# Kernel optimization log

Hardware: AMD Instinct MI355X
Metric: run time of the kernel (lower is better)

## Reference

```python
import jax, jax.numpy as jnp
import numpy as np

D = 1024
E = 8


def setup_inputs() -> dict:
    key = jax.random.key(0)
    ks = jax.random.split(key, 7)
    s = 1.0 / np.sqrt(D)
    x = jax.random.normal(ks[0], (4, 2048, D), dtype=jnp.float32)
    Wg = jax.random.uniform(ks[1], (D, E), minval=-s, maxval=s, dtype=jnp.float32)
    bg = jax.random.uniform(ks[2], (E,), minval=-s, maxval=s, dtype=jnp.float32)
    W1 = jax.random.uniform(ks[3], (E, D, D), minval=-s, maxval=s, dtype=jnp.float32)
    b1 = jax.random.uniform(ks[4], (E, D), minval=-s, maxval=s, dtype=jnp.float32)
    W2 = jax.random.uniform(ks[5], (E, D, D), minval=-s, maxval=s, dtype=jnp.float32)
    b2 = jax.random.uniform(ks[6], (E, D), minval=-s, maxval=s, dtype=jnp.float32)
    return {"x": x, "Wg": Wg, "bg": bg, "W1": W1, "b1": b1, "W2": W2, "b2": b2}


def reference(x, Wg, bg, W1, b1, W2, b2):
    N, T, d = x.shape
    x_flat = x.reshape(N * T, d)                                  # [NT, D]
    logits = x_flat @ Wg + bg                                     # [NT, E]
    probs = jax.nn.softmax(logits, axis=-1)
    assignments = jnp.argmax(probs, axis=-1)                      # [NT]
    # all-experts MLP (dense, as in the original module)
    h = jnp.einsum('nd,edh->neh', x_flat, W1) + b1[None]          # [NT, E, D]
    h = jax.nn.gelu(h, approximate=False)                         # torch GELU = exact erf
    eo = jnp.einsum('neh,ehd->ned', h, W2) + b2[None]             # [NT, E, D]
    selected = jnp.take_along_axis(eo, assignments[:, None, None], axis=1)[:, 0, :]  # [NT, D]
    w = jnp.take_along_axis(probs, assignments[:, None], axis=1)  # [NT, 1]
    out = (w * selected).reshape(N, T, d)
    return out
```

## Files before the change

### kernel.cpp

```cpp
#include <hip/hip_runtime.h>
#include <cstdint>

#define NT 8192
#define DD 1024
#define NE 8
#define BK 32
#define NKIT (DD / BK)
#define TM 64
#define MAXTILE 136

typedef __attribute__((ext_vector_type(8))) _Float16 half8;
typedef __attribute__((ext_vector_type(4))) float f32x4;

__device__ __forceinline__ unsigned short f2h_bits(float f) {
  _Float16 h = (_Float16)f;
  return __builtin_bit_cast(unsigned short, h);
}

#define GLDS16(gp, lp) __builtin_amdgcn_global_load_lds( \
  (__attribute__((address_space(1))) void*)(uintptr_t)(gp), \
  (__attribute__((address_space(3))) void*)(uintptr_t)(lp), 16, 0, 0)

#define WAITCNT_VM6  0xF76
#define WAITCNT_VM3  0xF73
#define WAITCNT_VM0  0xF70

__global__ __launch_bounds__(256) void wcast_kernel(
    const float* __restrict__ W1, const float* __restrict__ W2,
    _Float16* __restrict__ W1t, _Float16* __restrict__ W2t) {
  __shared__ float tile[64][65];
  const int z = blockIdx.z;
  const float* W = (z < 8 ? W1 : W2) + (size_t)(z & 7) * (DD * DD);
  _Float16* Wt   = (z < 8 ? W1t : W2t) + (size_t)(z & 7) * (DD * DD);
  const int k0 = blockIdx.x * 64, n0 = blockIdx.y * 64;
  const int tid = threadIdx.x;
#pragma unroll
  for (int it = 0; it < 4; ++it) {
    int idx = it * 256 + tid;
    int r = idx >> 4;
    int q = idx & 15;
    float4 v = *(const float4*)(W + (size_t)(k0 + r) * DD + n0 + q * 4);
    tile[r][q * 4 + 0] = v.x; tile[r][q * 4 + 1] = v.y;
    tile[r][q * 4 + 2] = v.z; tile[r][q * 4 + 3] = v.w;
  }
  __syncthreads();
#pragma unroll
  for (int it = 0; it < 4; ++it) {
    int idx = it * 256 + tid;
    int n = idx >> 4;
    int q = idx & 15;
    ushort4 o;
    o.x = f2h_bits(tile[q * 4 + 0][n]);
    o.y = f2h_bits(tile[q * 4 + 1][n]);
    o.z = f2h_bits(tile[q * 4 + 2][n]);
    o.w = f2h_bits(tile[q * 4 + 3][n]);
    *(ushort4*)(Wt + (size_t)(n0 + n) * DD + k0 + q * 4) = o;
  }
}

__global__ __launch_bounds__(256) void gate_kernel(
    const float* __restrict__ x, const float* __restrict__ Wg, const float* __restrict__ bg,
    int* __restrict__ assign, float* __restrict__ wgt, _Float16* __restrict__ xh) {
  __shared__ float WgL[NE * DD];
  const int tid = threadIdx.x;
#pragma unroll
  for (int it = 0; it < 8; ++it) {
    int idx = it * 256 + tid;
    float4 v = ((const float4*)Wg)[idx];
    int k = idx >> 1;
    int e0 = (idx & 1) * 4;
    WgL[(e0 + 0) * DD + k] = v.x;
    WgL[(e0 + 1) * DD + k] = v.y;
    WgL[(e0 + 2) * DD + k] = v.z;
    WgL[(e0 + 3) * DD + k] = v.w;
  }
  __syncthreads();
  const int lane = tid & 63, w = tid >> 6;
#pragma unroll
  for (int s = 0; s < 2; ++s) {
    const int t = blockIdx.x * 8 + w * 2 + s;
    const float4* xr = (const float4*)(x + (size_t)t * DD);
    float4 xv[4];
#pragma unroll
    for (int c = 0; c < 4; ++c) xv[c] = xr[lane + 64 * c];
    ushort4* xo = (ushort4*)(xh + (size_t)t * DD);
#pragma unroll
    for (int c = 0; c < 4; ++c) {
      union { ushort4 u; _Float16 h[4]; } cv;
      cv.h[0] = (_Float16)xv[c].x; cv.h[1] = (_Float16)xv[c].y;
      cv.h[2] = (_Float16)xv[c].z; cv.h[3] = (_Float16)xv[c].w;
      xo[lane + 64 * c] = cv.u;
    }
    float p[NE];
#pragma unroll
    for (int e = 0; e < NE; ++e) {
      float acc = 0.f;
#pragma unroll
      for (int c = 0; c < 4; ++c) {
        float4 wv = *(const float4*)&WgL[e * DD + 4 * lane + 256 * c];
        acc += xv[c].x * wv.x + xv[c].y * wv.y + xv[c].z * wv.z + xv[c].w * wv.w;
      }
      p[e] = acc;
    }
#pragma unroll
    for (int e = 0; e < NE; ++e) {
      float v = p[e];
      for (int off = 32; off > 0; off >>= 1) v += __shfl_down(v, off, 64);
      p[e] = v;
    }
    if (lane == 0) {
      float l[NE];
#pragma unroll
      for (int e = 0; e < NE; ++e) l[e] = p[e] + bg[e];
      int a = 0; float best = l[0];
#pragma unroll
      for (int e = 1; e < NE; ++e) if (l[e] > best) { best = l[e]; a = e; }
      float sum = 0.f;
#pragma unroll
      for (int e = 0; e < NE; ++e) sum += expf(l[e] - best);
      assign[t] = a;
      wgt[t] = 1.0f / sum;
    }
  }
}

__global__ __launch_bounds__(1024) void sort_kernel(
    const int* __restrict__ assign, int* __restrict__ rowtok, int* __restrict__ plan) {
  __shared__ int sc[NE * 1024];
  __shared__ int s_pref[NE + 1];
  const int tid = threadIdx.x;
  int a[8];
  int c[NE];
#pragma unroll
  for (int e = 0; e < NE; ++e) c[e] = 0;
#pragma unroll
  for (int j = 0; j < 8; ++j) { a[j] = assign[tid * 8 + j]; ++c[a[j]]; }
#pragma unroll
  for (int e = 0; e < NE; ++e) sc[e * 1024 + tid] = c[e];
  __syncthreads();
  for (int d = 1; d < 1024; d <<= 1) {
    int add[NE];
    if (tid >= d) {
#pragma unroll
      for (int e = 0; e < NE; ++e) add[e] = sc[e * 1024 + tid - d];
    }
    __syncthreads();
    if (tid >= d) {
#pragma unroll
      for (int e = 0; e < NE; ++e) sc[e * 1024 + tid] += add[e];
    }
    __syncthreads();
  }
  int tot[NE], incl[NE];
#pragma unroll
  for (int e = 0; e < NE; ++e) { tot[e] = sc[e * 1024 + 1023]; incl[e] = sc[e * 1024 + tid]; }
  int offs[NE];
  {
    int s = 0;
#pragma unroll
    for (int e = 0; e < NE; ++e) { offs[e] = s; s += tot[e]; }
  }
  int run[NE];
#pragma unroll
  for (int e = 0; e < NE; ++e) run[e] = offs[e] + incl[e] - c[e];
#pragma unroll
  for (int j = 0; j < 8; ++j) { int e = a[j]; rowtok[run[e]++] = tid * 8 + j; }
  if (tid == 0) {
    int s = 0;
    for (int e = 0; e < NE; ++e) { s_pref[e] = s; s += (tot[e] + TM - 1) / TM; }
    s_pref[NE] = s;
    plan[0] = s;
  }
  __syncthreads();
  const int nt = s_pref[NE];
  if (tid < nt) {
    int e = 0;
    while (tid >= s_pref[e + 1]) ++e;
    int t = tid - s_pref[e];
    plan[1 + tid] = e;
    plan[1 + MAXTILE + tid] = offs[e] + t * TM;
    plan[1 + 2 * MAXTILE + tid] = offs[e] + tot[e];
  }
}

template <int MODE>
__global__ __launch_bounds__(256) void gemm_kernel(
    const _Float16* __restrict__ A,
    const _Float16* __restrict__ Wt,
    const float* __restrict__ bias,
    const int* __restrict__ plan,
    _Float16* __restrict__ Hout,
    float* __restrict__ Fout,
    const int* __restrict__ rowtok,
    const float* __restrict__ wgt) {
  const int wrk = blockIdx.x;
  const int tile = wrk >> 3;
  if (tile >= plan[0]) return;
  const int e = plan[1 + tile];
  const int m0 = plan[1 + MAXTILE + tile];
  const int seg_end = plan[1 + 2 * MAXTILE + tile];
  const int n0 = (wrk & 7) * 128;

  const int tid = threadIdx.x;
  const int lane = tid & 63;
  const int wn = tid >> 6;
  const int quad = lane >> 4;
  const int r15 = lane & 15;

  __shared__ alignas(16) char lds[49152];

  const _Float16* We = Wt + (size_t)e * DD * DD;
  const _Float16* gAp;
  const _Float16* gBp[2];
  int ldsoA, ldsoB[2];
  {
    int slot = tid;
    int row = slot >> 2;
    int c = (slot & 3) ^ ((row >> 1) & 3);
    int rg = m0 + row; if (rg > NT - 1) rg = NT - 1;
    int arow = (MODE == 0) ? rowtok[rg] : rg;
    gAp = A + (size_t)arow * DD + c * 8;
    ldsoA = slot * 16;
  }
#pragma unroll
  for (int i = 0; i < 2; ++i) {
    int slot = i * 256 + tid;
    int row = slot >> 2;
    int c = (slot & 3) ^ ((row >> 1) & 3);
    gBp[i] = We + (size_t)(n0 + row) * DD + c * 8;
    ldsoB[i] = slot * 16;
  }

  int aoff[4], boff[2];
#pragma unroll
  for (int i = 0; i < 4; ++i) {
    int m = i * 16 + r15;
    aoff[i] = m * 4 + (quad ^ ((m >> 1) & 3));
  }
#pragma unroll
  for (int i = 0; i < 2; ++i) {
    int n = wn * 32 + i * 16 + r15;
    boff[i] = n * 4 + (quad ^ ((n >> 1) & 3));
  }

  f32x4 acc[4][2];
  f32x4 zero4 = {0.f, 0.f, 0.f, 0.f};
#pragma unroll
  for (int mi = 0; mi < 4; ++mi)
#pragma unroll
    for (int ni = 0; ni < 2; ++ni) acc[mi][ni] = zero4;

#define LDSBUF(B) (lds + (B) * 12288)
#define STAGE(KT, BUF) do {                                          \
    const int ko_ = (KT) * BK;                                       \
    char* lb_ = LDSBUF(BUF);                                         \
    GLDS16(gAp + ko_, lb_ + ldsoA);                                  \
    GLDS16(gBp[0] + ko_, lb_ + 4096 + ldsoB[0]);                     \
    GLDS16(gBp[1] + ko_, lb_ + 4096 + ldsoB[1]);                     \
  } while (0)
#define COMPUTE(BUF) do {                                            \
    const half8* AsV = (const half8*)(LDSBUF(BUF));                  \
    const half8* BsV = (const half8*)(LDSBUF(BUF) + 4096);           \
    half8 a_[4], b_[2];                                              \
    _Pragma("unroll")                                                \
    for (int i = 0; i < 4; ++i) a_[i] = AsV[aoff[i]];                \
    _Pragma("unroll")                                                \
    for (int i = 0; i < 2; ++i) b_[i] = BsV[boff[i]];                \
    _Pragma("unroll")                                                \
    for (int mi = 0; mi < 4; ++mi)                                   \
      _Pragma("unroll")                                              \
      for (int ni = 0; ni < 2; ++ni)                                 \
        acc[mi][ni] = __builtin_amdgcn_mfma_f32_16x16x32_f16(a_[mi], b_[ni], acc[mi][ni], 0, 0, 0); \
  } while (0)

  STAGE(0, 0);
  STAGE(1, 1);
  STAGE(2, 2);

#pragma unroll 1
  for (int kt = 0; kt < NKIT - 3; ++kt) {
    __builtin_amdgcn_s_waitcnt(WAITCNT_VM6);
    __builtin_amdgcn_s_barrier();
    __asm__ volatile("" ::: "memory");
    STAGE(kt + 3, (kt + 3) & 3);
    COMPUTE(kt & 3);
  }
  __builtin_amdgcn_s_waitcnt(WAITCNT_VM6);
  __builtin_amdgcn_s_barrier();
  __asm__ volatile("" ::: "memory");
  COMPUTE((NKIT - 3) & 3);
  __builtin_amdgcn_s_waitcnt(WAITCNT_VM3);
  __builtin_amdgcn_s_barrier();
  __asm__ volatile("" ::: "memory");
  COMPUTE((NKIT - 2) & 3);
  __builtin_amdgcn_s_waitcnt(WAITCNT_VM0);
  __builtin_amdgcn_s_barrier();
  __asm__ volatile("" ::: "memory");
  COMPUTE((NKIT - 1) & 3);
#undef COMPUTE
#undef STAGE
#undef LDSBUF

  const float* bptr = bias + (size_t)e * DD;
#pragma unroll
  for (int mi = 0; mi < 4; ++mi) {
    int rowb = m0 + mi * 16 + quad * 4;
#pragma unroll
    for (int r = 0; r < 4; ++r) {
      int gpos = rowb + r;
      if (gpos < seg_end) {
        if (MODE == 0) {
#pragma unroll
          for (int ni = 0; ni < 2; ++ni) {
            int n = n0 + wn * 32 + ni * 16 + r15;
            float val = acc[mi][ni][r] + bptr[n];
            val = 0.5f * val * (1.0f + erff(val * 0.70710678118654752f));
            Hout[(size_t)gpos * DD + n] = (_Float16)val;
          }
        } else {
          int tok = rowtok[gpos];
          float wv = wgt[tok];
          float* orow = Fout + (size_t)tok * DD;
#pragma unroll
          for (int ni = 0; ni < 2; ++ni) {
            int n = n0 + wn * 32 + ni * 16 + r15;
            orow[n] = (acc[mi][ni][r] + bptr[n]) * wv;
          }
        }
      }
    }
  }
}

extern "C" void kernel_launch(void* const* d_in, const int* in_sizes, int n_in,
                              void* d_out, int out_size, void* d_ws, size_t ws_size,
                              hipStream_t stream) {
  const float* x  = (const float*)d_in[0];
  const float* Wg = (const float*)d_in[1];
  const float* bg = (const float*)d_in[2];
  const float* W1 = (const float*)d_in[3];
  const float* b1 = (const float*)d_in[4];
  const float* W2 = (const float*)d_in[5];
  const float* b2 = (const float*)d_in[6];
  float* out = (float*)d_out;

  char* ws = (char*)d_ws;
  const size_t MB16 = (size_t)1 << 24;
  _Float16* W1t = (_Float16*)(ws + 0 * MB16);
  _Float16* W2t = (_Float16*)(ws + 1 * MB16);
  _Float16* xh  = (_Float16*)(ws + 2 * MB16);
  _Float16* H   = (_Float16*)(ws + 3 * MB16);
  int*   assign = (int*)(ws + 4 * MB16);
  int*   rowtok = assign + NT;
  float* wgt    = (float*)(rowtok + NT);
  int*   plan   = (int*)(wgt + NT);

  wcast_kernel<<<dim3(16, 16, 16), 256, 0, stream>>>(W1, W2, W1t, W2t);
  gate_kernel<<<NT / 8, 256, 0, stream>>>(x, Wg, bg, assign, wgt, xh);
  sort_kernel<<<1, 1024, 0, stream>>>(assign, rowtok, plan);
  gemm_kernel<0><<<MAXTILE * 8, 256, 0, stream>>>(xh, W1t, b1, plan, H, nullptr, rowtok, nullptr);
  gemm_kernel<1><<<MAXTILE * 8, 256, 0, stream>>>(H, W2t, b2, plan, nullptr, out, rowtok, wgt);
}
```

Measured before the change: 255.9 us.

## Split GEMM tile across 8 waves and use 3-stage LDS pipeline

Doubles the GEMM block to 512 threads so each wave computes a 32x32 sub-tile instead of 64x32, halving per-wave accumulators and A-fragment loads. The loads are split so every thread issues one B copy and the first 256 threads also issue one A copy. The LDS ring shrinks from 4 to 3 buffers, with the loop unrolled by three and per-wave waitcnt depths. This aims to add more waves for latency hiding and to lower the LDS footprint, at the cost of a shallower prefetch and uneven vmcnt bookkeeping between wave groups.

```diff
diff --git a/kernel.cpp b/kernel.cpp
--- a/kernel.cpp
+++ b/kernel.cpp
@@ -21,8 +21,8 @@
   (__attribute__((address_space(1))) void*)(uintptr_t)(gp), \
   (__attribute__((address_space(3))) void*)(uintptr_t)(lp), 16, 0, 0)
 
-#define WAITCNT_VM6  0xF76
-#define WAITCNT_VM3  0xF73
+#define WAITCNT_VM2  0xF72
+#define WAITCNT_VM1  0xF71
 #define WAITCNT_VM0  0xF70
 
 __global__ __launch_bounds__(256) void wcast_kernel(
@@ -184,7 +184,7 @@
 }
 
 template <int MODE>
-__global__ __launch_bounds__(256) void gemm_kernel(
+__global__ __launch_bounds__(512) void gemm_kernel(
     const _Float16* __restrict__ A,
     const _Float16* __restrict__ Wt,
     const float* __restrict__ bias,
@@ -203,17 +203,28 @@
 
   const int tid = threadIdx.x;
   const int lane = tid & 63;
-  const int wn = tid >> 6;
+  const int wv = tid >> 6;
+  const int wm = wv >> 2;
+  const int wq = wv & 3;
   const int quad = lane >> 4;
   const int r15 = lane & 15;
 
-  __shared__ alignas(16) char lds[49152];
+  __shared__ alignas(16) char lds[36864];
 
   const _Float16* We = Wt + (size_t)e * DD * DD;
-  const _Float16* gAp;
-  const _Float16* gBp[2];
-  int ldsoA, ldsoB[2];
+  const bool isA = (tid < 256);
+  const _Float16* gBp;
+  int ldsoB;
   {
+    int slot = tid;
+    int row = slot >> 2;
+    int c = (slot & 3) ^ ((row >> 1) & 3);
+    gBp = We + (size_t)(n0 + row) * DD + c * 8;
+    ldsoB = slot * 16;
+  }
+  const _Float16* gAp = A;
+  int ldsoA = 0;
+  if (isA) {
     int slot = tid;
     int row = slot >> 2;
     int c = (slot & 3) ^ ((row >> 1) & 3);
@@ -222,31 +233,24 @@
     gAp = A + (size_t)arow * DD + c * 8;
     ldsoA = slot * 16;
   }
+  const int wvu = __builtin_amdgcn_readfirstlane(wv);
+
+  int aoff[2], boff[2];
 #pragma unroll
   for (int i = 0; i < 2; ++i) {
-    int slot = i * 256 + tid;
-    int row = slot >> 2;
-    int c = (slot & 3) ^ ((row >> 1) & 3);
-    gBp[i] = We + (size_t)(n0 + row) * DD + c * 8;
-    ldsoB[i] = slot * 16;
-  }
-
-  int aoff[4], boff[2];
-#pragma unroll
-  for (int i = 0; i < 4; ++i) {
-    int m = i * 16 + r15;
+    int m = wm * 32 + i * 16 + r15;
     aoff[i] = m * 4 + (quad ^ ((m >> 1) & 3));
   }
 #pragma unroll
   for (int i = 0; i < 2; ++i) {
-    int n = wn * 32 + i * 16 + r15;
+    int n = wq * 32 + i * 16 + r15;
     boff[i] = n * 4 + (quad ^ ((n >> 1) & 3));
   }
 
-  f32x4 acc[4][2];
+  f32x4 acc[2][2];
   f32x4 zero4 = {0.f, 0.f, 0.f, 0.f};
 #pragma unroll
-  for (int mi = 0; mi < 4; ++mi)
+  for (int mi = 0; mi < 2; ++mi)
 #pragma unroll
     for (int ni = 0; ni < 2; ++ni) acc[mi][ni] = zero4;
 
@@ -254,57 +258,66 @@
 #define STAGE(KT, BUF) do {                                          \
     const int ko_ = (KT) * BK;                                       \
     char* lb_ = LDSBUF(BUF);                                         \
-    GLDS16(gAp + ko_, lb_ + ldsoA);                                  \
-    GLDS16(gBp[0] + ko_, lb_ + 4096 + ldsoB[0]);                     \
-    GLDS16(gBp[1] + ko_, lb_ + 4096 + ldsoB[1]);                     \
+    GLDS16(gBp + ko_, lb_ + 4096 + ldsoB);                           \
+    if (isA) GLDS16(gAp + ko_, lb_ + ldsoA);                         \
   } while (0)
 #define COMPUTE(BUF) do {                                            \
     const half8* AsV = (const half8*)(LDSBUF(BUF));                  \
     const half8* BsV = (const half8*)(LDSBUF(BUF) + 4096);           \
-    half8 a_[4], b_[2];                                              \
+    half8 a_[2], b_[2];                                              \
     _Pragma("unroll")                                                \
-    for (int i = 0; i < 4; ++i) a_[i] = AsV[aoff[i]];                \
+    for (int i = 0; i < 2; ++i) a_[i] = AsV[aoff[i]];                \
     _Pragma("unroll")                                                \
     for (int i = 0; i < 2; ++i) b_[i] = BsV[boff[i]];                \
     _Pragma("unroll")                                                \
-    for (int mi = 0; mi < 4; ++mi)                                   \
+    for (int mi = 0; mi < 2; ++mi)                                   \
       _Pragma("unroll")                                              \
       for (int ni = 0; ni < 2; ++ni)                                 \
         acc[mi][ni] = __builtin_amdgcn_mfma_f32_16x16x32_f16(a_[mi], b_[ni], acc[mi][ni], 0, 0, 0); \
   } while (0)
+#define WAIT_STEADY() do {                                           \
+    if (wvu < 4) __builtin_amdgcn_s_waitcnt(WAITCNT_VM2);            \
+    else         __builtin_amdgcn_s_waitcnt(WAITCNT_VM1);            \
+  } while (0)
 
   STAGE(0, 0);
   STAGE(1, 1);
-  STAGE(2, 2);
 
 #pragma unroll 1
-  for (int kt = 0; kt < NKIT - 3; ++kt) {
-    __builtin_amdgcn_s_waitcnt(WAITCNT_VM6);
+  for (int kt = 0; kt < NKIT - 2; kt += 3) {
+    WAIT_STEADY();
     __builtin_amdgcn_s_barrier();
     __asm__ volatile("" ::: "memory");
-    STAGE(kt + 3, (kt + 3) & 3);
-    COMPUTE(kt & 3);
-  }
-  __builtin_amdgcn_s_waitcnt(WAITCNT_VM6);
+    STAGE(kt + 2, 2);
+    COMPUTE(0);
+    WAIT_STEADY();
+    __builtin_amdgcn_s_barrier();
+    __asm__ volatile("" ::: "memory");
+    STAGE(kt + 3, 0);
+    COMPUTE(1);
+    WAIT_STEADY();
+    __builtin_amdgcn_s_barrier();
+    __asm__ volatile("" ::: "memory");
+    STAGE(kt + 4, 1);
+    COMPUTE(2);
+  }
+  WAIT_STEADY();
   __builtin_amdgcn_s_barrier();
   __asm__ volatile("" ::: "memory");
-  COMPUTE((NKIT - 3) & 3);
-  __builtin_amdgcn_s_waitcnt(WAITCNT_VM3);
-  __builtin_amdgcn_s_barrier();
-  __asm__ volatile("" ::: "memory");
-  COMPUTE((NKIT - 2) & 3);
+  COMPUTE(0);
   __builtin_amdgcn_s_waitcnt(WAITCNT_VM0);
   __builtin_amdgcn_s_barrier();
   __asm__ volatile("" ::: "memory");
-  COMPUTE((NKIT - 1) & 3);
+  COMPUTE(1);
+#undef WAIT_STEADY
 #undef COMPUTE
 #undef STAGE
 #undef LDSBUF
 
   const float* bptr = bias + (size_t)e * DD;
 #pragma unroll
-  for (int mi = 0; mi < 4; ++mi) {
-    int rowb = m0 + mi * 16 + quad * 4;
+  for (int mi = 0; mi < 2; ++mi) {
+    int rowb = m0 + wm * 32 + mi * 16 + quad * 4;
 #pragma unroll
     for (int r = 0; r < 4; ++r) {
       int gpos = rowb + r;
@@ -312,19 +325,19 @@
         if (MODE == 0) {
 #pragma unroll
           for (int ni = 0; ni < 2; ++ni) {
-            int n = n0 + wn * 32 + ni * 16 + r15;
+            int n = n0 + wq * 32 + ni * 16 + r15;
             float val = acc[mi][ni][r] + bptr[n];
             val = 0.5f * val * (1.0f + erff(val * 0.70710678118654752f));
             Hout[(size_t)gpos * DD + n] = (_Float16)val;
           }
         } else {
           int tok = rowtok[gpos];
-          float wv = wgt[tok];
+          float wgl = wgt[tok];
           float* orow = Fout + (size_t)tok * DD;
 #pragma unroll
           for (int ni = 0; ni < 2; ++ni) {
-            int n = n0 + wn * 32 + ni * 16 + r15;
-            orow[n] = (acc[mi][ni][r] + bptr[n]) * wv;
+            int n = n0 + wq * 32 + ni * 16 + r15;
+            orow[n] = (acc[mi][ni][r] + bptr[n]) * wgl;
           }
         }
       }
@@ -358,6 +371,6 @@
   wcast_kernel<<<dim3(16, 16, 16), 256, 0, stream>>>(W1, W2, W1t, W2t);
   gate_kernel<<<NT / 8, 256, 0, stream>>>(x, Wg, bg, assign, wgt, xh);
   sort_kernel<<<1, 1024, 0, stream>>>(assign, rowtok, plan);
-  gemm_kernel<0><<<MAXTILE * 8, 256, 0, stream>>>(xh, W1t, b1, plan, H, nullptr, rowtok, nullptr);
-  gemm_kernel<1><<<MAXTILE * 8, 256, 0, stream>>>(H, W2t, b2, plan, nullptr, out, rowtok, wgt);
-}
+  gemm_kernel<0><<<MAXTILE * 8, 512, 0, stream>>>(xh, W1t, b1, plan, H, nullptr, rowtok, nullptr);
+  gemm_kernel<1><<<MAXTILE * 8, 512, 0, stream>>>(H, W2t, b2, plan, nullptr, out, rowtok, wgt);
+}
```

After: 241.9 us. -5.4%, faster.

## Enlarge GEMM tiles to 128x128, triple-buffer pipeline, and merge prep kernels

Applied to the files above, without the earlier changes.

The grouped expert GEMMs move from 64x128 tiles with four waves each covering 64x32 to 128x128 tiles with a 2x2 wave grid, each wave computing 64x64. This raises MFMA work per LDS fragment load and halves the number of M tiles. The LDS pipeline goes from four stages to three 16KB buffers with the loop unrolled by three, and launch bounds ask for three blocks per CU. The weight-cast and gate kernels are merged into one launch to save a kernel launch. The larger M tile pads more rows per expert segment, fewer blocks may underfill the CUs, and the bigger accumulator set raises register pressure.

```diff
diff --git a/kernel.cpp b/kernel.cpp
--- a/kernel.cpp
+++ b/kernel.cpp
@@ -6,8 +6,8 @@
 #define NE 8
 #define BK 32
 #define NKIT (DD / BK)
-#define TM 64
-#define MAXTILE 136
+#define TM 128
+#define MAXTILE 72
 
 typedef __attribute__((ext_vector_type(8))) _Float16 half8;
 typedef __attribute__((ext_vector_type(4))) float f32x4;
@@ -21,105 +21,106 @@
   (__attribute__((address_space(1))) void*)(uintptr_t)(gp), \
   (__attribute__((address_space(3))) void*)(uintptr_t)(lp), 16, 0, 0)
 
-#define WAITCNT_VM6  0xF76
-#define WAITCNT_VM3  0xF73
+#define WAITCNT_VM4  0xF74
 #define WAITCNT_VM0  0xF70
 
-__global__ __launch_bounds__(256) void wcast_kernel(
+__global__ __launch_bounds__(256) void prep_kernel(
     const float* __restrict__ W1, const float* __restrict__ W2,
-    _Float16* __restrict__ W1t, _Float16* __restrict__ W2t) {
-  __shared__ float tile[64][65];
-  const int z = blockIdx.z;
-  const float* W = (z < 8 ? W1 : W2) + (size_t)(z & 7) * (DD * DD);
-  _Float16* Wt   = (z < 8 ? W1t : W2t) + (size_t)(z & 7) * (DD * DD);
-  const int k0 = blockIdx.x * 64, n0 = blockIdx.y * 64;
-  const int tid = threadIdx.x;
-#pragma unroll
-  for (int it = 0; it < 4; ++it) {
-    int idx = it * 256 + tid;
-    int r = idx >> 4;
-    int q = idx & 15;
-    float4 v = *(const float4*)(W + (size_t)(k0 + r) * DD + n0 + q * 4);
-    tile[r][q * 4 + 0] = v.x; tile[r][q * 4 + 1] = v.y;
-    tile[r][q * 4 + 2] = v.z; tile[r][q * 4 + 3] = v.w;
-  }
-  __syncthreads();
-#pragma unroll
-  for (int it = 0; it < 4; ++it) {
-    int idx = it * 256 + tid;
-    int n = idx >> 4;
-    int q = idx & 15;
-    ushort4 o;
-    o.x = f2h_bits(tile[q * 4 + 0][n]);
-    o.y = f2h_bits(tile[q * 4 + 1][n]);
-    o.z = f2h_bits(tile[q * 4 + 2][n]);
-    o.w = f2h_bits(tile[q * 4 + 3][n]);
-    *(ushort4*)(Wt + (size_t)(n0 + n) * DD + k0 + q * 4) = o;
-  }
-}
-
-__global__ __launch_bounds__(256) void gate_kernel(
+    _Float16* __restrict__ W1t, _Float16* __restrict__ W2t,
     const float* __restrict__ x, const float* __restrict__ Wg, const float* __restrict__ bg,
     int* __restrict__ assign, float* __restrict__ wgt, _Float16* __restrict__ xh) {
-  __shared__ float WgL[NE * DD];
+  __shared__ alignas(16) char smem[32768];
+  const int bid = blockIdx.x;
   const int tid = threadIdx.x;
-#pragma unroll
-  for (int it = 0; it < 8; ++it) {
-    int idx = it * 256 + tid;
-    float4 v = ((const float4*)Wg)[idx];
-    int k = idx >> 1;
-    int e0 = (idx & 1) * 4;
-    WgL[(e0 + 0) * DD + k] = v.x;
-    WgL[(e0 + 1) * DD + k] = v.y;
-    WgL[(e0 + 2) * DD + k] = v.z;
-    WgL[(e0 + 3) * DD + k] = v.w;
-  }
-  __syncthreads();
-  const int lane = tid & 63, w = tid >> 6;
-#pragma unroll
-  for (int s = 0; s < 2; ++s) {
-    const int t = blockIdx.x * 8 + w * 2 + s;
-    const float4* xr = (const float4*)(x + (size_t)t * DD);
-    float4 xv[4];
-#pragma unroll
-    for (int c = 0; c < 4; ++c) xv[c] = xr[lane + 64 * c];
-    ushort4* xo = (ushort4*)(xh + (size_t)t * DD);
-#pragma unroll
-    for (int c = 0; c < 4; ++c) {
-      union { ushort4 u; _Float16 h[4]; } cv;
-      cv.h[0] = (_Float16)xv[c].x; cv.h[1] = (_Float16)xv[c].y;
-      cv.h[2] = (_Float16)xv[c].z; cv.h[3] = (_Float16)xv[c].w;
-      xo[lane + 64 * c] = cv.u;
-    }
-    float p[NE];
-#pragma unroll
-    for (int e = 0; e < NE; ++e) {
-      float acc = 0.f;
+  if (bid < 4096) {
+    float (*tile)[65] = (float (*)[65])smem;
+    const int z = bid >> 8;
+    const float* W = (z < 8 ? W1 : W2) + (size_t)(z & 7) * (DD * DD);
+    _Float16* Wt   = (z < 8 ? W1t : W2t) + (size_t)(z & 7) * (DD * DD);
+    const int k0 = (bid & 15) * 64, n0 = ((bid >> 4) & 15) * 64;
+#pragma unroll
+    for (int it = 0; it < 4; ++it) {
+      int idx = it * 256 + tid;
+      int r = idx >> 4;
+      int q = idx & 15;
+      float4 v = *(const float4*)(W + (size_t)(k0 + r) * DD + n0 + q * 4);
+      tile[r][q * 4 + 0] = v.x; tile[r][q * 4 + 1] = v.y;
+      tile[r][q * 4 + 2] = v.z; tile[r][q * 4 + 3] = v.w;
+    }
+    __syncthreads();
+#pragma unroll
+    for (int it = 0; it < 4; ++it) {
+      int idx = it * 256 + tid;
+      int n = idx >> 4;
+      int q = idx & 15;
+      ushort4 o;
+      o.x = f2h_bits(tile[q * 4 + 0][n]);
+      o.y = f2h_bits(tile[q * 4 + 1][n]);
+      o.z = f2h_bits(tile[q * 4 + 2][n]);
+      o.w = f2h_bits(tile[q * 4 + 3][n]);
+      *(ushort4*)(Wt + (size_t)(n0 + n) * DD + k0 + q * 4) = o;
+    }
+  } else {
+    float* WgL = (float*)smem;
+    const int gb = bid - 4096;
+#pragma unroll
+    for (int it = 0; it < 8; ++it) {
+      int idx = it * 256 + tid;
+      float4 v = ((const float4*)Wg)[idx];
+      int k = idx >> 1;
+      int e0 = (idx & 1) * 4;
+      WgL[(e0 + 0) * DD + k] = v.x;
+      WgL[(e0 + 1) * DD + k] = v.y;
+      WgL[(e0 + 2) * DD + k] = v.z;
+      WgL[(e0 + 3) * DD + k] = v.w;
+    }
+    __syncthreads();
+    const int lane = tid & 63, w = tid >> 6;
+#pragma unroll
+    for (int s = 0; s < 2; ++s) {
+      const int t = gb * 8 + w * 2 + s;
+      const float4* xr = (const float4*)(x + (size_t)t * DD);
+      float4 xv[4];
+#pragma unroll
+      for (int c = 0; c < 4; ++c) xv[c] = xr[lane + 64 * c];
+      ushort4* xo = (ushort4*)(xh + (size_t)t * DD);
 #pragma unroll
       for (int c = 0; c < 4; ++c) {
-        float4 wv = *(const float4*)&WgL[e * DD + 4 * lane + 256 * c];
-        acc += xv[c].x * wv.x + xv[c].y * wv.y + xv[c].z * wv.z + xv[c].w * wv.w;
-      }
-      p[e] = acc;
-    }
-#pragma unroll
-    for (int e = 0; e < NE; ++e) {
-      float v = p[e];
-      for (int off = 32; off > 0; off >>= 1) v += __shfl_down(v, off, 64);
-      p[e] = v;
-    }
-    if (lane == 0) {
-      float l[NE];
-#pragma unroll
-      for (int e = 0; e < NE; ++e) l[e] = p[e] + bg[e];
-      int a = 0; float best = l[0];
-#pragma unroll
-      for (int e = 1; e < NE; ++e) if (l[e] > best) { best = l[e]; a = e; }
-      float sum = 0.f;
-#pragma unroll
-      for (int e = 0; e < NE; ++e) sum += expf(l[e] - best);
-      assign[t] = a;
-      wgt[t] = 1.0f / sum;
+        union { ushort4 u; _Float16 h[4]; } cv;
+        cv.h[0] = (_Float16)xv[c].x; cv.h[1] = (_Float16)xv[c].y;
+        cv.h[2] = (_Float16)xv[c].z; cv.h[3] = (_Float16)xv[c].w;
+        xo[lane + 64 * c] = cv.u;
+      }
+      float p[NE];
+#pragma unroll
+      for (int e = 0; e < NE; ++e) {
+        float acc = 0.f;
+#pragma unroll
+        for (int c = 0; c < 4; ++c) {
+          float4 wv = *(const float4*)&WgL[e * DD + 4 * lane + 256 * c];
+          acc += xv[c].x * wv.x + xv[c].y * wv.y + xv[c].z * wv.z + xv[c].w * wv.w;
+        }
+        p[e] = acc;
+      }
+#pragma unroll
+      for (int e = 0; e < NE; ++e) {
+        float v = p[e];
+        for (int off = 32; off > 0; off >>= 1) v += __shfl_down(v, off, 64);
+        p[e] = v;
+      }
+      if (lane == 0) {
+        float l[NE];
+#pragma unroll
+        for (int e = 0; e < NE; ++e) l[e] = p[e] + bg[e];
+        int a = 0; float best = l[0];
+#pragma unroll
+        for (int e = 1; e < NE; ++e) if (l[e] > best) { best = l[e]; a = e; }
+        float sum = 0.f;
+#pragma unroll
+        for (int e = 0; e < NE; ++e) sum += expf(l[e] - best);
+        assign[t] = a;
+        wgt[t] = 1.0f / sum;
+      }
     }
   }
 }
@@ -184,7 +185,7 @@
 }
 
 template <int MODE>
-__global__ __launch_bounds__(256) void gemm_kernel(
+__global__ __launch_bounds__(256, 3) void gemm_kernel(
     const _Float16* __restrict__ A,
     const _Float16* __restrict__ Wt,
     const float* __restrict__ bias,
@@ -203,100 +204,100 @@
 
   const int tid = threadIdx.x;
   const int lane = tid & 63;
-  const int wn = tid >> 6;
+  const int wv = tid >> 6;
+  const int wm = wv >> 1;
+  const int wq = wv & 1;
   const int quad = lane >> 4;
   const int r15 = lane & 15;
 
   __shared__ alignas(16) char lds[49152];
 
   const _Float16* We = Wt + (size_t)e * DD * DD;
-  const _Float16* gAp;
+  const _Float16* gAp[2];
   const _Float16* gBp[2];
-  int ldsoA, ldsoB[2];
-  {
-    int slot = tid;
+  int ldsoA[2], ldsoB[2];
+#pragma unroll
+  for (int i = 0; i < 2; ++i) {
+    int slot = i * 256 + tid;
     int row = slot >> 2;
     int c = (slot & 3) ^ ((row >> 1) & 3);
     int rg = m0 + row; if (rg > NT - 1) rg = NT - 1;
     int arow = (MODE == 0) ? rowtok[rg] : rg;
-    gAp = A + (size_t)arow * DD + c * 8;
-    ldsoA = slot * 16;
-  }
-#pragma unroll
-  for (int i = 0; i < 2; ++i) {
-    int slot = i * 256 + tid;
-    int row = slot >> 2;
-    int c = (slot & 3) ^ ((row >> 1) & 3);
+    gAp[i] = A + (size_t)arow * DD + c * 8;
+    ldsoA[i] = slot * 16;
     gBp[i] = We + (size_t)(n0 + row) * DD + c * 8;
     ldsoB[i] = slot * 16;
   }
 
-  int aoff[4], boff[2];
+  int aoff[4], boff[4];
 #pragma unroll
   for (int i = 0; i < 4; ++i) {
-    int m = i * 16 + r15;
+    int m = wm * 64 + i * 16 + r15;
     aoff[i] = m * 4 + (quad ^ ((m >> 1) & 3));
-  }
-#pragma unroll
-  for (int i = 0; i < 2; ++i) {
-    int n = wn * 32 + i * 16 + r15;
+    int n = wq * 64 + i * 16 + r15;
     boff[i] = n * 4 + (quad ^ ((n >> 1) & 3));
   }
 
-  f32x4 acc[4][2];
+  f32x4 acc[4][4];
   f32x4 zero4 = {0.f, 0.f, 0.f, 0.f};
 #pragma unroll
   for (int mi = 0; mi < 4; ++mi)
 #pragma unroll
-    for (int ni = 0; ni < 2; ++ni) acc[mi][ni] = zero4;
-
-#define LDSBUF(B) (lds + (B) * 12288)
+    for (int ni = 0; ni < 4; ++ni) acc[mi][ni] = zero4;
+
+#define LDSBUF(B) (lds + (B) * 16384)
 #define STAGE(KT, BUF) do {                                          \
     const int ko_ = (KT) * BK;                                       \
     char* lb_ = LDSBUF(BUF);                                         \
-    GLDS16(gAp + ko_, lb_ + ldsoA);                                  \
-    GLDS16(gBp[0] + ko_, lb_ + 4096 + ldsoB[0]);                     \
-    GLDS16(gBp[1] + ko_, lb_ + 4096 + ldsoB[1]);                     \
+    GLDS16(gAp[0] + ko_, lb_ + ldsoA[0]);                            \
+    GLDS16(gAp[1] + ko_, lb_ + ldsoA[1]);                            \
+    GLDS16(gBp[0] + ko_, lb_ + 8192 + ldsoB[0]);                     \
+    GLDS16(gBp[1] + ko_, lb_ + 8192 + ldsoB[1]);                     \
   } while (0)
 #define COMPUTE(BUF) do {                                            \
     const half8* AsV = (const half8*)(LDSBUF(BUF));                  \
-    const half8* BsV = (const half8*)(LDSBUF(BUF) + 4096);           \
-    half8 a_[4], b_[2];                                              \
+    const half8* BsV = (const half8*)(LDSBUF(BUF) + 8192);           \
+    half8 a_[4], b_[4];                                              \
     _Pragma("unroll")                                                \
     for (int i = 0; i < 4; ++i) a_[i] = AsV[aoff[i]];                \
     _Pragma("unroll")                                                \
-    for (int i = 0; i < 2; ++i) b_[i] = BsV[boff[i]];                \
+    for (int i = 0; i < 4; ++i) b_[i] = BsV[boff[i]];                \
     _Pragma("unroll")                                                \
     for (int mi = 0; mi < 4; ++mi)                                   \
       _Pragma("unroll")                                              \
-      for (int ni = 0; ni < 2; ++ni)                                 \
+      for (int ni = 0; ni < 4; ++ni)                                 \
         acc[mi][ni] = __builtin_amdgcn_mfma_f32_16x16x32_f16(a_[mi], b_[ni], acc[mi][ni], 0, 0, 0); \
   } while (0)
 
   STAGE(0, 0);
   STAGE(1, 1);
-  STAGE(2, 2);
 
 #pragma unroll 1
-  for (int kt = 0; kt < NKIT - 3; ++kt) {
-    __builtin_amdgcn_s_waitcnt(WAITCNT_VM6);
+  for (int kt = 0; kt < NKIT - 2; kt += 3) {
+    __builtin_amdgcn_s_waitcnt(WAITCNT_VM4);
     __builtin_amdgcn_s_barrier();
     __asm__ volatile("" ::: "memory");
-    STAGE(kt + 3, (kt + 3) & 3);
-    COMPUTE(kt & 3);
-  }
-  __builtin_amdgcn_s_waitcnt(WAITCNT_VM6);
+    STAGE(kt + 2, 2);
+    COMPUTE(0);
+    __builtin_amdgcn_s_waitcnt(WAITCNT_VM4);
+    __builtin_amdgcn_s_barrier();
+    __asm__ volatile("" ::: "memory");
+    STAGE(kt + 3, 0);
+    COMPUTE(1);
+    __builtin_amdgcn_s_waitcnt(WAITCNT_VM4);
+    __builtin_amdgcn_s_barrier();
+    __asm__ volatile("" ::: "memory");
+    STAGE(kt + 4, 1);
+    COMPUTE(2);
+  }
+  __builtin_amdgcn_s_waitcnt(WAITCNT_VM4);
   __builtin_amdgcn_s_barrier();
   __asm__ volatile("" ::: "memory");
-  COMPUTE((NKIT - 3) & 3);
-  __builtin_amdgcn_s_waitcnt(WAITCNT_VM3);
-  __builtin_amdgcn_s_barrier();
-  __asm__ volatile("" ::: "memory");
-  COMPUTE((NKIT - 2) & 3);
+  COMPUTE(0);
   __builtin_amdgcn_s_waitcnt(WAITCNT_VM0);
   __builtin_amdgcn_s_barrier();
   __asm__ volatile("" ::: "memory");
-  COMPUTE((NKIT - 1) & 3);
+  COMPUTE(1);
 #undef COMPUTE
 #undef STAGE
 #undef LDSBUF
@@ -304,27 +305,27 @@
   const float* bptr = bias + (size_t)e * DD;
 #pragma unroll
   for (int mi = 0; mi < 4; ++mi) {
-    int rowb = m0 + mi * 16 + quad * 4;
+    int rowb = m0 + wm * 64 + mi * 16 + quad * 4;
 #pragma unroll
     for (int r = 0; r < 4; ++r) {
       int gpos = rowb + r;
       if (gpos < seg_end) {
         if (MODE == 0) {
 #pragma unroll
-          for (int ni = 0; ni < 2; ++ni) {
-            int n = n0 + wn * 32 + ni * 16 + r15;
+          for (int ni = 0; ni < 4; ++ni) {
+            int n = n0 + wq * 64 + ni * 16 + r15;
             float val = acc[mi][ni][r] + bptr[n];
             val = 0.5f * val * (1.0f + erff(val * 0.70710678118654752f));
             Hout[(size_t)gpos * DD + n] = (_Float16)val;
           }
         } else {
           int tok = rowtok[gpos];
-          float wv = wgt[tok];
+          float wgl = wgt[tok];
           float* orow = Fout + (size_t)tok * DD;
 #pragma unroll
-          for (int ni = 0; ni < 2; ++ni) {
-            int n = n0 + wn * 32 + ni * 16 + r15;
-            orow[n] = (acc[mi][ni][r] + bptr[n]) * wv;
+          for (int ni = 0; ni < 4; ++ni) {
+            int n = n0 + wq * 64 + ni * 16 + r15;
+            orow[n] = (acc[mi][ni][r] + bptr[n]) * wgl;
           }
         }
       }
@@ -355,8 +356,7 @@
   float* wgt    = (float*)(rowtok + NT);
   int*   plan   = (int*)(wgt + NT);
 
-  wcast_kernel<<<dim3(16, 16, 16), 256, 0, stream>>>(W1, W2, W1t, W2t);
-  gate_kernel<<<NT / 8, 256, 0, stream>>>(x, Wg, bg, assign, wgt, xh);
+  prep_kernel<<<4096 + NT / 8, 256, 0, stream>>>(W1, W2, W1t, W2t, x, Wg, bg, assign, wgt, xh);
   sort_kernel<<<1, 1024, 0, stream>>>(assign, rowtok, plan);
   gemm_kernel<0><<<MAXTILE * 8, 256, 0, stream>>>(xh, W1t, b1, plan, H, nullptr, rowtok, nullptr);
   gemm_kernel<1><<<MAXTILE * 8, 256, 0, stream>>>(H, W2t, b2, plan, nullptr, out, rowtok, wgt);
```

After: 239.5 us. 6.4% less time.
